# Kernel optimization log

Measured on AMD Instinct MI355X. Metric: run time of the kernel, lower is better.

Reference implementation:

```python
import jax, jax.numpy as jnp
import numpy as np

N_NODES = 50000
NFEAT = 512
NHID = 128
N_EDGES = 800000
LN_EPS = 1e-5


def setup_inputs() -> dict:
    key = jax.random.key(0)
    k1, k2, k3, k4, k5 = jax.random.split(key, 5)
    h = jax.random.normal(k1, (N_NODES, NFEAT), dtype=jnp.float32)
    src = jax.random.randint(k2, (N_EDGES,), 0, N_NODES, dtype=jnp.int32)
    dst = jax.random.randint(k3, (N_EDGES,), 0, N_NODES, dtype=jnp.int32)
    # GraphConv params (glorot-ish) + bias; LayerNorm affine params
    W = jax.random.normal(k4, (NFEAT, NHID), dtype=jnp.float32) / np.sqrt(NFEAT)
    b = jnp.zeros((NHID,), dtype=jnp.float32)
    gamma = jnp.ones((NHID,), dtype=jnp.float32)
    beta = jnp.zeros((NHID,), dtype=jnp.float32)
    return {"h": h, "src": src, "dst": dst, "W": W, "b": b, "gamma": gamma, "beta": beta}


def reference(h, src, dst, W, b, gamma, beta):
    n = h.shape[0]
    ones = jnp.ones_like(src, dtype=jnp.float32)
    out_deg = jax.ops.segment_sum(ones, src, num_segments=n)
    in_deg = jax.ops.segment_sum(ones, dst, num_segments=n)
    out_norm = jnp.maximum(out_deg, 1.0) ** -0.5  # [N]
    in_norm = jnp.maximum(in_deg, 1.0) ** -0.5    # [N]

    # norm='both': scale source features by out_deg^{-1/2}
    x = h * out_norm[:, None]
    # in_feats > out_feats -> DGL multiplies by W before aggregation
    x = x @ W  # [N, NHID]
    # sparse aggregate: sum messages over incoming edges
    agg = jax.ops.segment_sum(x[src], dst, num_segments=n)  # [N, NHID]
    agg = agg * in_norm[:, None] + b

    # LayerNorm over last dim
    mu = jnp.mean(agg, axis=-1, keepdims=True)
    var = jnp.mean((agg - mu) ** 2, axis=-1, keepdims=True)
    y = (agg - mu) * jax.lax.rsqrt(var + LN_EPS) * gamma + beta
    return y
```

## Files before the change

### kernel.cpp

```cpp
#include <hip/hip_runtime.h>

#define N_NODES 50000
#define NFEAT   512
#define NHID    128
#define N_EDGES 800000
#define LN_EPS  1e-5f

#define GEMM_ROWS   32
#define GEMM_BLOCKS ((N_NODES + GEMM_ROWS - 1) / GEMM_ROWS)
#define DEG_BLOCKS  (N_EDGES / 256)

typedef __attribute__((ext_vector_type(8))) short bf16x8;
typedef __attribute__((ext_vector_type(4))) float fx4;

__device__ __forceinline__ unsigned short f2bf(float f) {
    union { float f; unsigned u; } v; v.f = f;
    unsigned r = v.u + 0x7FFF + ((v.u >> 16) & 1);
    return (unsigned short)(r >> 16);
}

__device__ __forceinline__ void bf2x(unsigned u, float& lo, float& hi) {
    union { unsigned u; float f; } a, b;
    a.u = u << 16;
    b.u = u & 0xFFFF0000u;
    lo = a.f; hi = b.f;
}

__global__ __launch_bounds__(256) void wprep_kernel(
    const float* __restrict__ W, unsigned short* __restrict__ wf)
{
    int tid = blockIdx.x * 256 + threadIdx.x;
    int lane = tid & 63;
    int frag = tid >> 6;
    int kc = frag >> 3, t = frag & 7;
    int n  = t * 16 + (lane & 15);
    int k0 = kc * 32 + (lane >> 4) * 8;
    unsigned short v[8];
#pragma unroll
    for (int j = 0; j < 8; j++)
        v[j] = f2bf(W[(size_t)(k0 + j) * NHID + n]);
    *(bf16x8*)(wf + (size_t)tid * 8) = *(bf16x8*)v;
}

__global__ __launch_bounds__(256) void fused_gemm_degree(
    const float* __restrict__ h, const unsigned short* __restrict__ wf,
    unsigned short* __restrict__ x,
    const int* __restrict__ src, const int* __restrict__ dst,
    int* __restrict__ out_deg, int* __restrict__ in_deg,
    int* __restrict__ edge_pos)
{
    __shared__ unsigned short afrag_lds[2][16 * 64 * 8];

    const int tid = threadIdx.x;
    const int B = blockIdx.x;
    bool isDeg; int id;
    if (B < 2 * GEMM_BLOCKS) { isDeg = (B & 1); id = B >> 1; }
    else                     { isDeg = true;    id = B - GEMM_BLOCKS; }

    if (isDeg) {
        int e = id * 256 + tid;
        int s = src[e];
        int d = dst[e];
        int pos = atomicAdd(&in_deg[d], 1);
        atomicAdd(&out_deg[s], 1);
        edge_pos[e] = pos;
        return;
    }

    const int row0 = id * GEMM_ROWS;

#pragma unroll
    for (int it = 0; it < 16; it++) {
        int i = tid + it * 256;
        int r  = i >> 7;
        int grow = row0 + r;
        if (grow > N_NODES - 1) grow = N_NODES - 1;
        float4 v = ((const float4*)h)[(size_t)grow * 128 + (i & 127)];
        int g  = r >> 4;
        int rr = r & 15;
        int k0 = (i & 127) << 2;
        int kc = k0 >> 5;
        int q  = (k0 >> 3) & 3;
        int j  = k0 & 7;
        unsigned long long pk =
            (unsigned long long)f2bf(v.x)
          | ((unsigned long long)f2bf(v.y) << 16)
          | ((unsigned long long)f2bf(v.z) << 32)
          | ((unsigned long long)f2bf(v.w) << 48);
        *(unsigned long long*)(&afrag_lds[g][0] + kc * 512 + (q * 16 + rr) * 8 + j) = pk;
    }
    __syncthreads();

    const int wave = tid >> 6;
    const int lane = tid & 63;
    const int t0   = wave * 2;

    fx4 acc00 = (fx4){0.f, 0.f, 0.f, 0.f};
    fx4 acc01 = (fx4){0.f, 0.f, 0.f, 0.f};
    fx4 acc10 = (fx4){0.f, 0.f, 0.f, 0.f};
    fx4 acc11 = (fx4){0.f, 0.f, 0.f, 0.f};

    const bf16x8* a0p = (const bf16x8*)&afrag_lds[0][0] + lane;
    const bf16x8* a1p = (const bf16x8*)&afrag_lds[1][0] + lane;
    const bf16x8* wfp = (const bf16x8*)wf + t0 * 64 + lane;

#pragma unroll 4
    for (int kc = 0; kc < 16; kc++) {
        bf16x8 a0 = a0p[kc * 64];
        bf16x8 a1 = a1p[kc * 64];
        bf16x8 b0 = wfp[kc * 512];
        bf16x8 b1 = wfp[kc * 512 + 64];
        acc00 = __builtin_amdgcn_mfma_f32_16x16x32_bf16(a0, b0, acc00, 0, 0, 0);
        acc01 = __builtin_amdgcn_mfma_f32_16x16x32_bf16(a0, b1, acc01, 0, 0, 0);
        acc10 = __builtin_amdgcn_mfma_f32_16x16x32_bf16(a1, b0, acc10, 0, 0, 0);
        acc11 = __builtin_amdgcn_mfma_f32_16x16x32_bf16(a1, b1, acc11, 0, 0, 0);
    }

    const int q = lane >> 4;
    const int c = lane & 15;
#pragma unroll
    for (int reg = 0; reg < 4; reg++) {
        int r0 = row0 + q * 4 + reg;
        if (r0 < N_NODES) {
            unsigned short* xr = x + (size_t)r0 * NHID;
            xr[t0 * 16 + c]       = f2bf(acc00[reg]);
            xr[(t0 + 1) * 16 + c] = f2bf(acc01[reg]);
        }
        int r1 = row0 + 16 + q * 4 + reg;
        if (r1 < N_NODES) {
            unsigned short* xr = x + (size_t)r1 * NHID;
            xr[t0 * 16 + c]       = f2bf(acc10[reg]);
            xr[(t0 + 1) * 16 + c] = f2bf(acc11[reg]);
        }
    }
}

__global__ __launch_bounds__(1024) void scan_local(
    const int* __restrict__ in_deg, int* __restrict__ row_ptr, int* __restrict__ bsum)
{
    __shared__ int wsum[16];
    const int tid = threadIdx.x;
    const int lane = tid & 63, wave = tid >> 6;
    int i = blockIdx.x * 1024 + tid;
    int v = (i < N_NODES) ? in_deg[i] : 0;
    int sv = v;
#pragma unroll
    for (int off = 1; off < 64; off <<= 1) {
        int t = __shfl_up(sv, off);
        if (lane >= off) sv += t;
    }
    if (lane == 63) wsum[wave] = sv;
    __syncthreads();
    if (wave == 0) {
        int wv = (lane < 16) ? wsum[lane] : 0;
#pragma unroll
        for (int off = 1; off < 16; off <<= 1) {
            int t = __shfl_up(wv, off);
            if (lane >= off) wv += t;
        }
        if (lane < 16) wsum[lane] = wv;
    }
    __syncthreads();
    int excl = ((wave > 0) ? wsum[wave - 1] : 0) + (sv - v);
    if (i < N_NODES) row_ptr[i] = excl;
    if (tid == 1023) bsum[blockIdx.x] = wsum[15];
}

__global__ __launch_bounds__(64) void scan_bsums(int* __restrict__ bsum, int* __restrict__ row_ptr)
{
    const int lane = threadIdx.x;
    const int nb = (N_NODES + 1023) / 1024;
    int v = (lane < nb) ? bsum[lane] : 0;
    int sv = v;
#pragma unroll
    for (int off = 1; off < 64; off <<= 1) {
        int t = __shfl_up(sv, off);
        if (lane >= off) sv += t;
    }
    if (lane < nb) bsum[lane] = sv - v;
    if (lane == 63) row_ptr[N_NODES] = sv;
}

__global__ __launch_bounds__(1024) void scan_add(
    int* __restrict__ row_ptr, const int* __restrict__ bsum,
    const int* __restrict__ out_deg, float* __restrict__ out_norm)
{
    int i = blockIdx.x * 1024 + threadIdx.x;
    if (i < N_NODES) {
        if (blockIdx.x > 0) row_ptr[i] += bsum[blockIdx.x];
        out_norm[i] = rsqrtf(fmaxf((float)out_deg[i], 1.0f));
    }
}

__global__ __launch_bounds__(256) void fill_kernel(
    const int* __restrict__ src, const int* __restrict__ dst,
    const int* __restrict__ row_ptr, const int* __restrict__ edge_pos,
    int* __restrict__ csr_src)
{
    int e = blockIdx.x * 256 + threadIdx.x;
    if (e < N_EDGES) {
        int d = dst[e];
        csr_src[row_ptr[d] + edge_pos[e]] = src[e];
    }
}

__global__ __launch_bounds__(256) void aggregate_kernel(
    const unsigned short* __restrict__ x, const int* __restrict__ row_ptr,
    const int* __restrict__ csr_src, const float* __restrict__ out_norm,
    const float* __restrict__ b, const float* __restrict__ gamma,
    const float* __restrict__ beta, float* __restrict__ out)
{
    const int n    = blockIdx.x * 4 + (threadIdx.x >> 6);
    const int lane = threadIdx.x & 63;
    const int half = lane >> 5;
    const int c    = lane & 31;
    const int start = row_ptr[n];
    const int end   = row_ptr[n + 1];

    float a0 = 0.f, a1 = 0.f, a2 = 0.f, a3 = 0.f;

    for (int base = start; base < end; base += 64) {
        int me   = base + lane;
        int msrc = (me < end) ? csr_src[me] : 0;
        int cnt  = min(64, end - base);
        int npair = (cnt + 1) >> 1;
        int j = 0;
        for (; j + 4 <= npair; j += 4) {
            int i0 = 2 * j + half, i1 = i0 + 2, i2 = i0 + 4, i3 = i0 + 6;
            int s0 = __shfl(msrc, i0);
            int s1 = __shfl(msrc, i1);
            int s2 = __shfl(msrc, i2);
            int s3 = __shfl(msrc, i3);
            float w0 = (i0 < cnt) ? out_norm[s0] : 0.f;
            float w1 = (i1 < cnt) ? out_norm[s1] : 0.f;
            float w2 = (i2 < cnt) ? out_norm[s2] : 0.f;
            float w3 = (i3 < cnt) ? out_norm[s3] : 0.f;
            uint2 u0 = *(const uint2*)(x + (size_t)s0 * NHID + c * 4);
            uint2 u1 = *(const uint2*)(x + (size_t)s1 * NHID + c * 4);
            uint2 u2 = *(const uint2*)(x + (size_t)s2 * NHID + c * 4);
            uint2 u3 = *(const uint2*)(x + (size_t)s3 * NHID + c * 4);
            float p0, p1, p2, p3;
            bf2x(u0.x, p0, p1); bf2x(u0.y, p2, p3);
            a0 += p0 * w0; a1 += p1 * w0; a2 += p2 * w0; a3 += p3 * w0;
            bf2x(u1.x, p0, p1); bf2x(u1.y, p2, p3);
            a0 += p0 * w1; a1 += p1 * w1; a2 += p2 * w1; a3 += p3 * w1;
            bf2x(u2.x, p0, p1); bf2x(u2.y, p2, p3);
            a0 += p0 * w2; a1 += p1 * w2; a2 += p2 * w2; a3 += p3 * w2;
            bf2x(u3.x, p0, p1); bf2x(u3.y, p2, p3);
            a0 += p0 * w3; a1 += p1 * w3; a2 += p2 * w3; a3 += p3 * w3;
        }
        for (; j < npair; ++j) {
            int i0 = 2 * j + half;
            int s0 = __shfl(msrc, i0);
            float w0 = (i0 < cnt) ? out_norm[s0] : 0.f;
            uint2 u0 = *(const uint2*)(x + (size_t)s0 * NHID + c * 4);
            float p0, p1, p2, p3;
            bf2x(u0.x, p0, p1); bf2x(u0.y, p2, p3);
            a0 += p0 * w0; a1 += p1 * w0; a2 += p2 * w0; a3 += p3 * w0;
        }
    }

    a0 += __shfl_xor(a0, 32);
    a1 += __shfl_xor(a1, 32);
    a2 += __shfl_xor(a2, 32);
    a3 += __shfl_xor(a3, 32);

    float inorm = rsqrtf(fmaxf((float)(end - start), 1.0f));
    float4 bb = *(const float4*)(b + c * 4);
    float v0 = a0 * inorm + bb.x;
    float v1 = a1 * inorm + bb.y;
    float v2 = a2 * inorm + bb.z;
    float v3 = a3 * inorm + bb.w;

    float s = v0 + v1 + v2 + v3;
#pragma unroll
    for (int off = 16; off > 0; off >>= 1) s += __shfl_xor(s, off);
    float mu = s * (1.0f / 128.0f);

    float d0 = v0 - mu, d1 = v1 - mu, d2 = v2 - mu, d3 = v3 - mu;
    float qd = d0 * d0 + d1 * d1 + d2 * d2 + d3 * d3;
#pragma unroll
    for (int off = 16; off > 0; off >>= 1) qd += __shfl_xor(qd, off);
    float var = qd * (1.0f / 128.0f);
    float rs = rsqrtf(var + LN_EPS);

    if (half == 0) {
        float4 gg = *(const float4*)(gamma + c * 4);
        float4 be = *(const float4*)(beta + c * 4);
        float4 o;
        o.x = d0 * rs * gg.x + be.x;
        o.y = d1 * rs * gg.y + be.y;
        o.z = d2 * rs * gg.z + be.z;
        o.w = d3 * rs * gg.w + be.w;
        *(float4*)(out + (size_t)n * NHID + c * 4) = o;
    }
}

extern "C" void kernel_launch(void* const* d_in, const int* in_sizes, int n_in,
                              void* d_out, int out_size, void* d_ws, size_t ws_size,
                              hipStream_t stream) {
    const float* h     = (const float*)d_in[0];
    const int*   src   = (const int*)d_in[1];
    const int*   dst   = (const int*)d_in[2];
    const float* W     = (const float*)d_in[3];
    const float* b     = (const float*)d_in[4];
    const float* gamma = (const float*)d_in[5];
    const float* beta  = (const float*)d_in[6];
    float* out = (float*)d_out;

    char* ws = (char*)d_ws;
    const size_t DEG_BYTES = 200704;
    const size_t RP_BYTES  = 200960;
    int*            out_deg  = (int*)(ws);
    int*            in_deg   = (int*)(ws + DEG_BYTES);
    int*            row_ptr  = (int*)(ws + 2 * DEG_BYTES);
    float*          out_norm = (float*)(ws + 2 * DEG_BYTES + RP_BYTES);
    int*            bsum     = (int*)(ws + 3 * DEG_BYTES + RP_BYTES);
    int*            edge_pos = (int*)(ws + 3 * DEG_BYTES + RP_BYTES + 1024);
    int*            csr_src  = (int*)(ws + 3 * DEG_BYTES + RP_BYTES + 1024 + (size_t)N_EDGES * 4);
    unsigned short* wf       = (unsigned short*)(ws + 3 * DEG_BYTES + RP_BYTES + 1024 + 2 * (size_t)N_EDGES * 4);
    unsigned short* x        = (unsigned short*)(ws + 3 * DEG_BYTES + RP_BYTES + 1024 + 2 * (size_t)N_EDGES * 4 + 131072);

    hipMemsetAsync(d_ws, 0, 2 * DEG_BYTES, stream);

    const int NB = (N_NODES + 1023) / 1024;
    wprep_kernel<<<32, 256, 0, stream>>>(W, wf);
    fused_gemm_degree<<<GEMM_BLOCKS + DEG_BLOCKS, 256, 0, stream>>>(
        h, wf, x, src, dst, out_deg, in_deg, edge_pos);
    scan_local  <<<NB, 1024, 0, stream>>>(in_deg, row_ptr, bsum);
    scan_bsums  <<<1, 64, 0, stream>>>(bsum, row_ptr);
    scan_add    <<<NB, 1024, 0, stream>>>(row_ptr, bsum, out_deg, out_norm);
    fill_kernel <<<(N_EDGES + 255) / 256, 256, 0, stream>>>(src, dst, row_ptr, edge_pos, csr_src);
    aggregate_kernel<<<N_NODES / 4, 256, 0, stream>>>(
        x, row_ptr, csr_src, out_norm, b, gamma, beta, out);
}
```

Measured before the change: 257.2 us.

## Fuse memset into prep, merge scan kernels, swizzle GEMM LDS layout

Replaces the hipMemsetAsync of the degree arrays with zeroing inside a combined W-prep kernel. It folds the block-sum scan into the scan-add kernel, so each block rescans the small bsum array itself, and moves the out_norm computation into scan_local. This removes two launches and one memset. It also XOR-swizzles the A-fragment LDS layout in the GEMM to cut bank conflicts on the stores and loads. The cost is redundant per-block rescans of bsum and slightly more index arithmetic.

```diff
diff --git a/kernel.cpp b/kernel.cpp
--- a/kernel.cpp
+++ b/kernel.cpp
@@ -9,6 +9,7 @@
 #define GEMM_ROWS   32
 #define GEMM_BLOCKS ((N_NODES + GEMM_ROWS - 1) / GEMM_ROWS)
 #define DEG_BLOCKS  (N_EDGES / 256)
+#define NB_SCAN     ((N_NODES + 1023) / 1024)
 
 typedef __attribute__((ext_vector_type(8))) short bf16x8;
 typedef __attribute__((ext_vector_type(4))) float fx4;
@@ -26,20 +27,27 @@
     lo = a.f; hi = b.f;
 }
 
-__global__ __launch_bounds__(256) void wprep_kernel(
-    const float* __restrict__ W, unsigned short* __restrict__ wf)
-{
-    int tid = blockIdx.x * 256 + threadIdx.x;
-    int lane = tid & 63;
-    int frag = tid >> 6;
-    int kc = frag >> 3, t = frag & 7;
-    int n  = t * 16 + (lane & 15);
-    int k0 = kc * 32 + (lane >> 4) * 8;
-    unsigned short v[8];
-#pragma unroll
-    for (int j = 0; j < 8; j++)
-        v[j] = f2bf(W[(size_t)(k0 + j) * NHID + n]);
-    *(bf16x8*)(wf + (size_t)tid * 8) = *(bf16x8*)v;
+__global__ __launch_bounds__(256) void prep_kernel(
+    const float* __restrict__ W, unsigned short* __restrict__ wf,
+    int4* __restrict__ zero_ptr)
+{
+    int t = blockIdx.x * 256 + threadIdx.x;
+#pragma unroll
+    for (int i = t; i < 25088; i += 16384)
+        zero_ptr[i] = make_int4(0, 0, 0, 0);
+
+    if (blockIdx.x < 32) {
+        int lane = t & 63;
+        int frag = t >> 6;
+        int kc = frag >> 3, tt = frag & 7;
+        int n  = tt * 16 + (lane & 15);
+        int k0 = kc * 32 + (lane >> 4) * 8;
+        unsigned short v[8];
+#pragma unroll
+        for (int j = 0; j < 8; j++)
+            v[j] = f2bf(W[(size_t)(k0 + j) * NHID + n]);
+        *(bf16x8*)(wf + (size_t)t * 8) = *(bf16x8*)v;
+    }
 }
 
 __global__ __launch_bounds__(256) void fused_gemm_degree(
@@ -82,32 +90,38 @@
         int kc = k0 >> 5;
         int q  = (k0 >> 3) & 3;
         int j  = k0 & 7;
+        int gp = q * 16 + (rr ^ (q | ((kc & 1) << 2)));
         unsigned long long pk =
             (unsigned long long)f2bf(v.x)
           | ((unsigned long long)f2bf(v.y) << 16)
           | ((unsigned long long)f2bf(v.z) << 32)
           | ((unsigned long long)f2bf(v.w) << 48);
-        *(unsigned long long*)(&afrag_lds[g][0] + kc * 512 + (q * 16 + rr) * 8 + j) = pk;
+        *(unsigned long long*)(&afrag_lds[g][0] + kc * 512 + gp * 8 + j) = pk;
     }
     __syncthreads();
 
     const int wave = tid >> 6;
     const int lane = tid & 63;
     const int t0   = wave * 2;
+    const int rr_l = lane & 15;
+    const int q_l  = lane >> 4;
+    const int g_e  = q_l * 16 + (rr_l ^ q_l);
+    const int g_o  = q_l * 16 + (rr_l ^ q_l ^ 4);
 
     fx4 acc00 = (fx4){0.f, 0.f, 0.f, 0.f};
     fx4 acc01 = (fx4){0.f, 0.f, 0.f, 0.f};
     fx4 acc10 = (fx4){0.f, 0.f, 0.f, 0.f};
     fx4 acc11 = (fx4){0.f, 0.f, 0.f, 0.f};
 
-    const bf16x8* a0p = (const bf16x8*)&afrag_lds[0][0] + lane;
-    const bf16x8* a1p = (const bf16x8*)&afrag_lds[1][0] + lane;
+    const bf16x8* a0p = (const bf16x8*)&afrag_lds[0][0];
+    const bf16x8* a1p = (const bf16x8*)&afrag_lds[1][0];
     const bf16x8* wfp = (const bf16x8*)wf + t0 * 64 + lane;
 
 #pragma unroll 4
     for (int kc = 0; kc < 16; kc++) {
-        bf16x8 a0 = a0p[kc * 64];
-        bf16x8 a1 = a1p[kc * 64];
+        int gidx = (kc & 1) ? g_o : g_e;
+        bf16x8 a0 = a0p[kc * 64 + gidx];
+        bf16x8 a1 = a1p[kc * 64 + gidx];
         bf16x8 b0 = wfp[kc * 512];
         bf16x8 b1 = wfp[kc * 512 + 64];
         acc00 = __builtin_amdgcn_mfma_f32_16x16x32_bf16(a0, b0, acc00, 0, 0, 0);
@@ -136,7 +150,8 @@
 }
 
 __global__ __launch_bounds__(1024) void scan_local(
-    const int* __restrict__ in_deg, int* __restrict__ row_ptr, int* __restrict__ bsum)
+    const int* __restrict__ in_deg, int* __restrict__ row_ptr, int* __restrict__ bsum,
+    const int* __restrict__ out_deg, float* __restrict__ out_norm)
 {
     __shared__ int wsum[16];
     const int tid = threadIdx.x;
@@ -150,6 +165,8 @@
         if (lane >= off) sv += t;
     }
     if (lane == 63) wsum[wave] = sv;
+    if (i < N_NODES)
+        out_norm[i] = rsqrtf(fmaxf((float)out_deg[i], 1.0f));
     __syncthreads();
     if (wave == 0) {
         int wv = (lane < 16) ? wsum[lane] : 0;
@@ -166,30 +183,30 @@
     if (tid == 1023) bsum[blockIdx.x] = wsum[15];
 }
 
-__global__ __launch_bounds__(64) void scan_bsums(int* __restrict__ bsum, int* __restrict__ row_ptr)
-{
-    const int lane = threadIdx.x;
-    const int nb = (N_NODES + 1023) / 1024;
-    int v = (lane < nb) ? bsum[lane] : 0;
-    int sv = v;
-#pragma unroll
-    for (int off = 1; off < 64; off <<= 1) {
-        int t = __shfl_up(sv, off);
-        if (lane >= off) sv += t;
-    }
-    if (lane < nb) bsum[lane] = sv - v;
-    if (lane == 63) row_ptr[N_NODES] = sv;
-}
-
-__global__ __launch_bounds__(1024) void scan_add(
-    int* __restrict__ row_ptr, const int* __restrict__ bsum,
-    const int* __restrict__ out_deg, float* __restrict__ out_norm)
-{
-    int i = blockIdx.x * 1024 + threadIdx.x;
-    if (i < N_NODES) {
-        if (blockIdx.x > 0) row_ptr[i] += bsum[blockIdx.x];
-        out_norm[i] = rsqrtf(fmaxf((float)out_deg[i], 1.0f));
-    }
+__global__ __launch_bounds__(1024) void scan_add2(
+    int* __restrict__ row_ptr, const int* __restrict__ bsum)
+{
+    __shared__ int off_s, tot_s;
+    const int tid = threadIdx.x;
+    if (tid < 64) {
+        int v = (tid < NB_SCAN) ? bsum[tid] : 0;
+        int sv = v;
+#pragma unroll
+        for (int off = 1; off < 64; off <<= 1) {
+            int t = __shfl_up(sv, off);
+            if (tid >= off) sv += t;
+        }
+        int pre = __shfl(sv, (blockIdx.x == 0) ? 0 : (blockIdx.x - 1));
+        int tot = __shfl(sv, NB_SCAN - 1);
+        if (tid == 0) {
+            off_s = (blockIdx.x == 0) ? 0 : pre;
+            tot_s = tot;
+        }
+    }
+    __syncthreads();
+    int i = blockIdx.x * 1024 + tid;
+    if (i < N_NODES) row_ptr[i] += off_s;
+    if (blockIdx.x == 0 && tid == 0) row_ptr[N_NODES] = tot_s;
 }
 
 __global__ __launch_bounds__(256) void fill_kernel(
@@ -321,16 +338,12 @@
     unsigned short* wf       = (unsigned short*)(ws + 3 * DEG_BYTES + RP_BYTES + 1024 + 2 * (size_t)N_EDGES * 4);
     unsigned short* x        = (unsigned short*)(ws + 3 * DEG_BYTES + RP_BYTES + 1024 + 2 * (size_t)N_EDGES * 4 + 131072);
 
-    hipMemsetAsync(d_ws, 0, 2 * DEG_BYTES, stream);
-
-    const int NB = (N_NODES + 1023) / 1024;
-    wprep_kernel<<<32, 256, 0, stream>>>(W, wf);
+    prep_kernel<<<64, 256, 0, stream>>>(W, wf, (int4*)ws);
     fused_gemm_degree<<<GEMM_BLOCKS + DEG_BLOCKS, 256, 0, stream>>>(
         h, wf, x, src, dst, out_deg, in_deg, edge_pos);
-    scan_local  <<<NB, 1024, 0, stream>>>(in_deg, row_ptr, bsum);
-    scan_bsums  <<<1, 64, 0, stream>>>(bsum, row_ptr);
-    scan_add    <<<NB, 1024, 0, stream>>>(row_ptr, bsum, out_deg, out_norm);
-    fill_kernel <<<(N_EDGES + 255) / 256, 256, 0, stream>>>(src, dst, row_ptr, edge_pos, csr_src);
+    scan_local<<<NB_SCAN, 1024, 0, stream>>>(in_deg, row_ptr, bsum, out_deg, out_norm);
+    scan_add2 <<<NB_SCAN, 1024, 0, stream>>>(row_ptr, bsum);
+    fill_kernel<<<(N_EDGES + 255) / 256, 256, 0, stream>>>(src, dst, row_ptr, edge_pos, csr_src);
     aggregate_kernel<<<N_NODES / 4, 256, 0, stream>>>(
         x, row_ptr, csr_src, out_norm, b, gamma, beta, out);
 }
```

After: 255.4 us. No clear change (-0.7%).
